# Kernel tuning notes

Hardware: AMD Instinct MI355X
Metric: run time of the kernel (lower is better)

The kernel has to match this reference:

```python
import jax, jax.numpy as jnp
from jax import lax
import numpy as np

B, S, V, C, H, Z, NSTEP = 256, 128, 128, 16, 1024, 256, 128
VC = V * C


def _gru_cell(x, h, Wih, Whh, bih, bhh):
    # torch GRUCell: gates ordered r, z, n along rows of (3H, in)
    gi = x @ Wih.T + bih
    gh = h @ Whh.T + bhh
    ir, iz, inn = jnp.split(gi, 3, axis=-1)
    hr, hz, hn = jnp.split(gh, 3, axis=-1)
    r = jax.nn.sigmoid(ir + hr)
    zg = jax.nn.sigmoid(iz + hz)
    n = jnp.tanh(inn + r * hn)
    return (1.0 - zg) * n + zg * h


def setup_inputs() -> dict:
    key = jax.random.key(0)
    ks = jax.random.split(key, 32)
    sc = 0.05
    p = lambda k, shape: (jax.random.normal(k, shape, jnp.float32) * sc)
    inp = {
        "x": jax.random.normal(ks[0], (B, V, S), jnp.float32),
        "noise": jax.random.normal(ks[1], (B, Z), jnp.float32),
        "gruf_Wih": p(ks[2], (3 * H, V)), "gruf_Whh": p(ks[3], (3 * H, H)),
        "gruf_bih": p(ks[4], (3 * H,)), "gruf_bhh": p(ks[5], (3 * H,)),
        "grub_Wih": p(ks[6], (3 * H, V)), "grub_Whh": p(ks[7], (3 * H, H)),
        "grub_bih": p(ks[8], (3 * H,)), "grub_bhh": p(ks[9], (3 * H,)),
        "Wmu": p(ks[10], (Z, 2 * H)), "bmu": p(ks[11], (Z,)),
        "Wvar": p(ks[12], (Z, 2 * H)), "bvar": p(ks[13], (Z,)),
        "Winit": p(ks[14], (H, Z)), "binit": p(ks[15], (H,)),
        "c1_Wih": p(ks[16], (3 * H, Z + VC)), "c1_Whh": p(ks[17], (3 * H, H)),
        "c1_bih": p(ks[18], (3 * H,)), "c1_bhh": p(ks[19], (3 * H,)),
        "c2_Wih": p(ks[20], (3 * H, H)), "c2_Whh": p(ks[21], (3 * H, H)),
        "c2_bih": p(ks[22], (3 * H,)), "c2_bhh": p(ks[23], (3 * H,)),
        "Wout": p(ks[24], (VC, H)), "bout": p(ks[25], (VC,)),
    }
    return inp


def reference(x, noise, gruf_Wih, gruf_Whh, gruf_bih, gruf_bhh,
              grub_Wih, grub_Whh, grub_bih, grub_bhh,
              Wmu, bmu, Wvar, bvar, Winit, binit,
              c1_Wih, c1_Whh, c1_bih, c1_bhh,
              c2_Wih, c2_Whh, c2_bih, c2_bhh, Wout, bout):
    b = x.shape[0]
    xe = jnp.transpose(x, (0, 2, 1))           # (b, s, V)
    xt = jnp.swapaxes(xe, 0, 1)                # (s, b, V) time-major
    h0 = jnp.zeros((b, H), x.dtype)

    def step_f(h, xs):
        h2 = _gru_cell(xs, h, gruf_Wih, gruf_Whh, gruf_bih, gruf_bhh)
        return h2, None

    def step_b(h, xs):
        h2 = _gru_cell(xs, h, grub_Wih, grub_Whh, grub_bih, grub_bhh)
        return h2, None

    hf, _ = lax.scan(step_f, h0, xt)
    hb, _ = lax.scan(step_b, h0, xt[::-1])
    enc = jnp.concatenate([hf, hb], axis=-1)   # (b, 2H) = h_n transposed+flattened

    mu = enc @ Wmu.T + bmu
    var = jnp.exp(enc @ Wvar.T + bvar)         # Normal(mu, var): var is the scale
    z = mu + var * noise                       # rsample

    out0 = jnp.zeros((b, VC), x.dtype).at[:, -1].set(1.0)
    h1_0 = jnp.tanh(z @ Winit.T + binit)
    h2_0 = jnp.zeros((b, H), x.dtype)

    def dstep(carry, i):
        out, h1, h2 = carry
        inp = jnp.concatenate([out, z], axis=1)          # (b, VC + Z)
        h1n = _gru_cell(inp, h1, c1_Wih, c1_Whh, c1_bih, c1_bhh)
        h2_prev = jnp.where(i == 0, h1n, h2)             # hx[1] = hx[0] at step 0
        h2n = _gru_cell(h1n, h2_prev, c2_Wih, c2_Whh, c2_bih, c2_bhh)
        logits = h2n @ Wout.T + bout                     # (b, VC)
        ls = jax.nn.log_softmax(logits.reshape(b, C, V), axis=1).reshape(b, VC)
        # eval-mode _sampling: argmax -> one-hot (no gradient flows through it)
        out_n = jax.nn.one_hot(jnp.argmax(ls, axis=1), VC, dtype=ls.dtype)
        return (out_n, h1n, h2n), ls

    _, xs = lax.scan(dstep, (out0, h1_0, h2_0), jnp.arange(NSTEP))
    recon_seq = jnp.swapaxes(xs, 0, 1)                   # (b, n_step, VC)
    recon = jnp.transpose(recon_seq, (0, 2, 1)).reshape(b, C, V, NSTEP)
    return mu, var, z, recon
```

## Files before the change

### kernel.cpp

```cpp
#include <hip/hip_runtime.h>
#include <cstdint>
#include <cstddef>

typedef __attribute__((ext_vector_type(8))) short bf16x8;
typedef __attribute__((ext_vector_type(4))) float f32x4;

#define DEVI __device__ __forceinline__

constexpr int B = 256, S = 128, V = 128, C = 16, H = 1024, Z = 256, NSTEP = 128;
constexpr int VC = V * C;
constexpr int G3 = 3 * H;

DEVI unsigned short f2bf(float f) {
  unsigned u = __float_as_uint(f);
  u += 0x7fffu + ((u >> 16) & 1u);
  return (unsigned short)(u >> 16);
}
DEVI float sigm(float x) { return 1.0f / (1.0f + expf(-x)); }

__global__ void k_cvt(const float* __restrict__ src, unsigned short* __restrict__ dst, int n) {
  for (int i = blockIdx.x * 256 + threadIdx.x; i < n; i += gridDim.x * 256)
    dst[i] = f2bf(src[i]);
}

__global__ void k_xt(const float* __restrict__ x, unsigned short* __restrict__ xtb) {
  __shared__ float tile[32][33];
  int sb = blockIdx.x * 32, rb = blockIdx.y * 32;
  int tx = threadIdx.x, ty = threadIdx.y;
  for (int i = ty; i < 32; i += 8) tile[i][tx] = x[(size_t)(rb + i) * S + sb + tx];
  __syncthreads();
  for (int i = ty; i < 32; i += 8)
    xtb[(size_t)(sb + i) * (B * V) + rb + tx] = f2bf(tile[tx][i]);
}

__global__ void k_wt(const float* __restrict__ w, float* __restrict__ wt) {
  __shared__ float tile[32][33];
  int vb = blockIdx.x * 32, nb = blockIdx.y * 32;
  int tx = threadIdx.x, ty = threadIdx.y;
  for (int i = ty; i < 32; i += 8) tile[i][tx] = w[(size_t)(nb + i) * (VC + Z) + vb + tx];
  __syncthreads();
  for (int i = ty; i < 32; i += 8)
    wt[(size_t)(vb + i) * G3 + nb + tx] = tile[tx][i];
}

struct GemmJob {
  const unsigned short* A;
  const unsigned short* Bw;
  float* Cm;
  int lda, ldb, ldc, K;
};
struct GemmJobs4 { GemmJob j[4]; };

typedef __attribute__((address_space(1))) const unsigned short* gas_p;
typedef __attribute__((address_space(3))) unsigned short* las_p;

__global__ __launch_bounds__(256) void k_gemm(GemmJobs4 jobs) {
  GemmJob jb = jobs.j[blockIdx.z];
  const int tid = threadIdx.x;
  const int wave = tid >> 6;
  const int lane = tid & 63;
  const int bn = blockIdx.x * 64;
  const int bm = blockIdx.y * 64;
  __shared__ unsigned short As[64 * 64];
  __shared__ unsigned short Bs[64 * 64];
  f32x4 acc[2][2] = {};
  const int wm = ((wave >> 1) & 1) * 32;
  const int wn = (wave & 1) * 32;
  const int rrow = (lane >> 3) & 7;
  const int pc = lane & 7;
  const int l15 = lane & 15;
  const int l4 = lane >> 4;

  const int nkt = jb.K >> 6;
  for (int kt = 0; kt < nkt; ++kt) {
    const int kbase = kt << 6;
    __syncthreads();
#pragma unroll
    for (int i = 0; i < 2; ++i) {
      int row = wave * 16 + i * 8 + rrow;
      int c = pc ^ (row & 7);
      const unsigned short* ga = jb.A + (size_t)(bm + row) * jb.lda + kbase + c * 8;
      __builtin_amdgcn_global_load_lds((gas_p)ga, (las_p)&As[(wave * 16 + i * 8) * 64], 16, 0, 0);
      const unsigned short* gb = jb.Bw + (size_t)(bn + row) * jb.ldb + kbase + c * 8;
      __builtin_amdgcn_global_load_lds((gas_p)gb, (las_p)&Bs[(wave * 16 + i * 8) * 64], 16, 0, 0);
    }
    __syncthreads();
#pragma unroll
    for (int kf = 0; kf < 2; ++kf) {
      int ch = (kf << 2) + l4;
      bf16x8 af[2], bfr[2];
#pragma unroll
      for (int mi = 0; mi < 2; ++mi) {
        int row = wm + mi * 16 + l15;
        af[mi] = *(const bf16x8*)&As[row * 64 + ((ch ^ (row & 7)) << 3)];
      }
#pragma unroll
      for (int ni = 0; ni < 2; ++ni) {
        int row = wn + ni * 16 + l15;
        bfr[ni] = *(const bf16x8*)&Bs[row * 64 + ((ch ^ (row & 7)) << 3)];
      }
#pragma unroll
      for (int mi = 0; mi < 2; ++mi)
#pragma unroll
        for (int ni = 0; ni < 2; ++ni)
          acc[mi][ni] = __builtin_amdgcn_mfma_f32_16x16x32_bf16(af[mi], bfr[ni], acc[mi][ni], 0, 0, 0);
    }
  }
#pragma unroll
  for (int mi = 0; mi < 2; ++mi)
#pragma unroll
    for (int ni = 0; ni < 2; ++ni) {
      int m0 = bm + wm + mi * 16 + l4 * 4;
      int n0 = bn + wn + ni * 16 + l15;
#pragma unroll
      for (int r = 0; r < 4; ++r)
        jb.Cm[(size_t)(m0 + r) * jb.ldc + n0] = acc[mi][ni][r];
    }
}

__global__ void k_enc_combine(const float* __restrict__ gif, const float* __restrict__ ghf,
                              const float* __restrict__ gib, const float* __restrict__ ghb,
                              const float* __restrict__ bihf, const float* __restrict__ bhhf,
                              const float* __restrict__ bihb, const float* __restrict__ bhhb,
                              float* __restrict__ hf, unsigned short* __restrict__ hfb,
                              float* __restrict__ hb, unsigned short* __restrict__ hbb) {
  int idx = blockIdx.x * 256 + threadIdx.x;
  int b = idx >> 10, jj = idx & (H - 1);
  const float *gi, *gh, *bih, *bhh; float* h; unsigned short* hB;
  if (blockIdx.y == 0) { gi = gif; gh = ghf; bih = bihf; bhh = bhhf; h = hf; hB = hfb; }
  else                 { gi = gib; gh = ghb; bih = bihb; bhh = bhhb; h = hb; hB = hbb; }
  int base = b * G3 + jj;
  float ir = gi[base] + bih[jj];
  float iz = gi[base + H] + bih[H + jj];
  float in_ = gi[base + 2 * H] + bih[2 * H + jj];
  float hr = gh[base] + bhh[jj];
  float hz = gh[base + H] + bhh[H + jj];
  float hn = gh[base + 2 * H] + bhh[2 * H + jj];
  float r = sigm(ir + hr);
  float zg = sigm(iz + hz);
  float n = tanhf(in_ + r * hn);
  float hnew = (1.f - zg) * n + zg * h[idx];
  h[idx] = hnew;
  hB[idx] = f2bf(hnew);
}

__global__ void k_combine1(const float* __restrict__ zpart, const float* __restrict__ WT,
                           const float* __restrict__ gh1, const float* __restrict__ bhh,
                           const int* __restrict__ idxb,
                           float* __restrict__ h1, unsigned short* __restrict__ h1b) {
  int idx = blockIdx.x * 256 + threadIdx.x;
  int b = idx >> 10, jj = idx & (H - 1);
  const float* wrow = WT + (size_t)idxb[b] * G3;
  int base = b * G3 + jj;
  float ir = zpart[base] + wrow[jj];
  float iz = zpart[base + H] + wrow[H + jj];
  float in_ = zpart[base + 2 * H] + wrow[2 * H + jj];
  float hr = gh1[base] + bhh[jj];
  float hz = gh1[base + H] + bhh[H + jj];
  float hn = gh1[base + 2 * H] + bhh[2 * H + jj];
  float r = sigm(ir + hr);
  float zg = sigm(iz + hz);
  float n = tanhf(in_ + r * hn);
  float hnew = (1.f - zg) * n + zg * h1[idx];
  h1[idx] = hnew;
  h1b[idx] = f2bf(hnew);
}

__global__ void k_combine2(const float* __restrict__ gi2, const float* __restrict__ gh2,
                           const float* __restrict__ bih, const float* __restrict__ bhh,
                           const float* __restrict__ h2prev,
                           float* __restrict__ h2, unsigned short* __restrict__ h2b) {
  int idx = blockIdx.x * 256 + threadIdx.x;
  int b = idx >> 10, jj = idx & (H - 1);
  int base = b * G3 + jj;
  float ir = gi2[base] + bih[jj];
  float iz = gi2[base + H] + bih[H + jj];
  float in_ = gi2[base + 2 * H] + bih[2 * H + jj];
  float hr = gh2[base] + bhh[jj];
  float hz = gh2[base + H] + bhh[H + jj];
  float hn = gh2[base + 2 * H] + bhh[2 * H + jj];
  float r = sigm(ir + hr);
  float zg = sigm(iz + hz);
  float n = tanhf(in_ + r * hn);
  float hnew = (1.f - zg) * n + zg * h2prev[idx];
  h2[idx] = hnew;
  h2b[idx] = f2bf(hnew);
}

__global__ __launch_bounds__(256) void k_mu_var_z(const float* __restrict__ hf, const float* __restrict__ hb,
                                                  const float* __restrict__ Wmu, const float* __restrict__ bmu,
                                                  const float* __restrict__ Wvar, const float* __restrict__ bvar,
                                                  const float* __restrict__ noise,
                                                  float* __restrict__ omu, float* __restrict__ ovar,
                                                  float* __restrict__ oz, float* __restrict__ zws) {
  __shared__ float e[2 * H];
  int b = blockIdx.x, t = threadIdx.x;
  for (int i = 0; i < 2 * H / 256; ++i) {
    int k = t + i * 256;
    e[k] = (k < H) ? hf[b * H + k] : hb[b * H + k - H];
  }
  __syncthreads();
  const float* wm = Wmu + (size_t)t * 2 * H;
  const float* wv = Wvar + (size_t)t * 2 * H;
  float am = bmu[t], av = bvar[t];
  for (int k = 0; k < 2 * H; ++k) { am += e[k] * wm[k]; av += e[k] * wv[k]; }
  float vv = expf(av);
  float zz = am + vv * noise[b * Z + t];
  omu[b * Z + t] = am; ovar[b * Z + t] = vv; oz[b * Z + t] = zz; zws[b * Z + t] = zz;
}

__global__ void k_zpart(const float* __restrict__ z, const float* __restrict__ c1Wih,
                        const float* __restrict__ bih, float* __restrict__ zpart) {
  int idx = blockIdx.x * 256 + threadIdx.x;
  int b = idx / G3, n = idx % G3;
  const float* w = c1Wih + (size_t)n * (VC + Z) + VC;
  const float* zr = z + b * Z;
  float a = bih[n];
  for (int k = 0; k < Z; ++k) a += zr[k] * w[k];
  zpart[idx] = a;
}

__global__ void k_h1init(const float* __restrict__ z, const float* __restrict__ Winit,
                         const float* __restrict__ binit,
                         float* __restrict__ h1, unsigned short* __restrict__ h1b,
                         int* __restrict__ idxb) {
  int idx = blockIdx.x * 256 + threadIdx.x;
  int b = idx >> 10, jj = idx & (H - 1);
  const float* w = Winit + (size_t)jj * Z;
  const float* zr = z + b * Z;
  float a = binit[jj];
  for (int k = 0; k < Z; ++k) a += zr[k] * w[k];
  float t = tanhf(a);
  h1[idx] = t; h1b[idx] = f2bf(t);
  if (idx < B) idxb[idx] = VC - 1;
}

__global__ __launch_bounds__(256) void k_softmax(const float* __restrict__ logits,
                                                 const float* __restrict__ bout,
                                                 float* __restrict__ lsbuf, int slot,
                                                 int* __restrict__ idxb) {
  int b = blockIdx.x, t = threadIdx.x;
  __shared__ float ls[VC];
  __shared__ float rv[256];
  __shared__ int ri[256];
  for (int i = 0; i < VC / 256; ++i) {
    int n = t + i * 256;
    ls[n] = logits[(size_t)b * VC + n] + bout[n];
  }
  __syncthreads();
  if (t < V) {
    float m = -1e30f;
    for (int c = 0; c < C; ++c) m = fmaxf(m, ls[c * V + t]);
    float s = 0.f;
    for (int c = 0; c < C; ++c) s += expf(ls[c * V + t] - m);
    float lse = m + logf(s);
    for (int c = 0; c < C; ++c) ls[c * V + t] -= lse;
  }
  __syncthreads();
  float bv = -1e30f; int bi = 0;
  for (int i = 0; i < VC / 256; ++i) {
    int n = i * 256 + t;
    float v = ls[n];
    if (v > bv) { bv = v; bi = n; }
  }
  rv[t] = bv; ri[t] = bi;
  __syncthreads();
  for (int s2 = 128; s2 > 0; s2 >>= 1) {
    if (t < s2) {
      float v2 = rv[t + s2]; int i2 = ri[t + s2];
      if (v2 > rv[t] || (v2 == rv[t] && i2 < ri[t])) { rv[t] = v2; ri[t] = i2; }
    }
    __syncthreads();
  }
  if (t == 0) idxb[b] = ri[0];
  float* dst = lsbuf + (size_t)slot * B * VC + (size_t)b * VC;
  for (int i = 0; i < VC / 256; ++i) { int n = t + i * 256; dst[n] = ls[n]; }
}

__global__ void k_flush(const float* __restrict__ lsbuf, float* __restrict__ recon, int t0) {
  int idx = blockIdx.x * 256 + threadIdx.x;
  float* dst = recon + (size_t)idx * NSTEP + t0;
#pragma unroll
  for (int j = 0; j < 16; ++j) dst[j] = lsbuf[(size_t)j * B * VC + idx];
}

extern "C" void kernel_launch(void* const* d_in, const int* in_sizes, int n_in,
                              void* d_out, int out_size, void* d_ws, size_t ws_size,
                              hipStream_t stream) {
  const float* x        = (const float*)d_in[0];
  const float* noise    = (const float*)d_in[1];
  const float* gruf_Wih = (const float*)d_in[2];
  const float* gruf_Whh = (const float*)d_in[3];
  const float* gruf_bih = (const float*)d_in[4];
  const float* gruf_bhh = (const float*)d_in[5];
  const float* grub_Wih = (const float*)d_in[6];
  const float* grub_Whh = (const float*)d_in[7];
  const float* grub_bih = (const float*)d_in[8];
  const float* grub_bhh = (const float*)d_in[9];
  const float* Wmu      = (const float*)d_in[10];
  const float* bmu      = (const float*)d_in[11];
  const float* Wvar     = (const float*)d_in[12];
  const float* bvar     = (const float*)d_in[13];
  const float* Winit    = (const float*)d_in[14];
  const float* binit    = (const float*)d_in[15];
  const float* c1_Wih   = (const float*)d_in[16];
  const float* c1_Whh   = (const float*)d_in[17];
  const float* c1_bih   = (const float*)d_in[18];
  const float* c1_bhh   = (const float*)d_in[19];
  const float* c2_Wih   = (const float*)d_in[20];
  const float* c2_Whh   = (const float*)d_in[21];
  const float* c2_bih   = (const float*)d_in[22];
  const float* c2_bhh   = (const float*)d_in[23];
  const float* Wout     = (const float*)d_in[24];
  const float* bout     = (const float*)d_in[25];

  float* omu = (float*)d_out;
  float* ovar = omu + B * Z;
  float* oz = ovar + B * Z;
  float* orecon = oz + B * Z;

  char* p = (char*)d_ws;
  auto carve = [&](size_t bytes) { char* r = p; p += (bytes + 255) & ~(size_t)255; return r; };
  unsigned short* wihf_b  = (unsigned short*)carve((size_t)G3 * V * 2);
  unsigned short* whhf_b  = (unsigned short*)carve((size_t)G3 * H * 2);
  unsigned short* wihb_b  = (unsigned short*)carve((size_t)G3 * V * 2);
  unsigned short* whhb_b  = (unsigned short*)carve((size_t)G3 * H * 2);
  unsigned short* wc1hh_b = (unsigned short*)carve((size_t)G3 * H * 2);
  unsigned short* wc2ih_b = (unsigned short*)carve((size_t)G3 * H * 2);
  unsigned short* wc2hh_b = (unsigned short*)carve((size_t)G3 * H * 2);
  unsigned short* wout_b  = (unsigned short*)carve((size_t)VC * H * 2);
  unsigned short* xtb     = (unsigned short*)carve((size_t)S * B * V * 2);
  unsigned short* hfb     = (unsigned short*)carve((size_t)B * H * 2);
  unsigned short* hbb     = (unsigned short*)carve((size_t)B * H * 2);
  unsigned short* h1b     = (unsigned short*)carve((size_t)B * H * 2);
  unsigned short* h2b     = (unsigned short*)carve((size_t)B * H * 2);
  float* WT     = (float*)carve((size_t)VC * G3 * 4);
  float* zpart  = (float*)carve((size_t)B * G3 * 4);
  float* g0     = (float*)carve((size_t)B * G3 * 4);
  float* g1     = (float*)carve((size_t)B * G3 * 4);
  float* g2     = (float*)carve((size_t)B * G3 * 4);
  float* g3     = (float*)carve((size_t)B * G3 * 4);
  float* hf     = (float*)carve((size_t)B * H * 4);
  float* hb     = (float*)carve((size_t)B * H * 4);
  float* h1     = (float*)carve((size_t)B * H * 4);
  float* h2     = (float*)carve((size_t)B * H * 4);
  float* zws    = (float*)carve((size_t)B * Z * 4);
  float* logits = (float*)carve((size_t)B * VC * 4);
  float* lsbuf  = (float*)carve((size_t)16 * B * VC * 4);
  int* idxb     = (int*)carve((size_t)B * 4);

  dim3 blk(256);

  auto cvt = [&](const float* s, unsigned short* d, int n) {
    int nb = (n + 255) / 256; if (nb > 2048) nb = 2048;
    k_cvt<<<nb, blk, 0, stream>>>(s, d, n);
  };
  cvt(gruf_Wih, wihf_b, G3 * V);
  cvt(gruf_Whh, whhf_b, G3 * H);
  cvt(grub_Wih, wihb_b, G3 * V);
  cvt(grub_Whh, whhb_b, G3 * H);
  cvt(c1_Whh, wc1hh_b, G3 * H);
  cvt(c2_Wih, wc2ih_b, G3 * H);
  cvt(c2_Whh, wc2hh_b, G3 * H);
  cvt(Wout, wout_b, VC * H);
  k_xt<<<dim3(S / 32, (B * V) / 32), dim3(32, 8), 0, stream>>>(x, xtb);
  k_wt<<<dim3(VC / 32, G3 / 32), dim3(32, 8), 0, stream>>>(c1_Wih, WT);

  hipMemsetAsync(hf, 0, (size_t)B * H * 4, stream);
  hipMemsetAsync(hb, 0, (size_t)B * H * 4, stream);
  hipMemsetAsync(hfb, 0, (size_t)B * H * 2, stream);
  hipMemsetAsync(hbb, 0, (size_t)B * H * 2, stream);

  for (int s = 0; s < S; ++s) {
    GemmJobs4 jj;
    jj.j[0] = { xtb + (size_t)s * B * V,           wihf_b, g0, V, V, G3, V };
    jj.j[1] = { hfb,                               whhf_b, g1, H, H, G3, H };
    jj.j[2] = { xtb + (size_t)(S - 1 - s) * B * V, wihb_b, g2, V, V, G3, V };
    jj.j[3] = { hbb,                               whhb_b, g3, H, H, G3, H };
    k_gemm<<<dim3(G3 / 64, B / 64, 4), blk, 0, stream>>>(jj);
    k_enc_combine<<<dim3(B * H / 256, 2), blk, 0, stream>>>(
        g0, g1, g2, g3, gruf_bih, gruf_bhh, grub_bih, grub_bhh, hf, hfb, hb, hbb);
  }

  k_mu_var_z<<<B, blk, 0, stream>>>(hf, hb, Wmu, bmu, Wvar, bvar, noise, omu, ovar, oz, zws);
  k_zpart<<<B * G3 / 256, blk, 0, stream>>>(zws, c1_Wih, c1_bih, zpart);
  k_h1init<<<B * H / 256, blk, 0, stream>>>(zws, Winit, binit, h1, h1b, idxb);

  for (int t = 0; t < NSTEP; ++t) {
    GemmJobs4 ja;
    ja.j[0] = { h1b, wc1hh_b, g0, H, H, G3, H };
    ja.j[1] = ja.j[0]; ja.j[2] = ja.j[0]; ja.j[3] = ja.j[0];
    k_gemm<<<dim3(G3 / 64, B / 64, 1), blk, 0, stream>>>(ja);
    k_combine1<<<B * H / 256, blk, 0, stream>>>(zpart, WT, g0, c1_bhh, idxb, h1, h1b);

    GemmJobs4 jc;
    jc.j[0] = { h1b,                     wc2ih_b, g1, H, H, G3, H };
    jc.j[1] = { (t == 0 ? h1b : h2b),    wc2hh_b, g2, H, H, G3, H };
    jc.j[2] = jc.j[0]; jc.j[3] = jc.j[0];
    k_gemm<<<dim3(G3 / 64, B / 64, 2), blk, 0, stream>>>(jc);
    k_combine2<<<B * H / 256, blk, 0, stream>>>(g1, g2, c2_bih, c2_bhh,
                                                (t == 0 ? h1 : h2), h2, h2b);

    GemmJobs4 jl;
    jl.j[0] = { h2b, wout_b, logits, H, H, VC, H };
    jl.j[1] = jl.j[0]; jl.j[2] = jl.j[0]; jl.j[3] = jl.j[0];
    k_gemm<<<dim3(VC / 64, B / 64, 1), blk, 0, stream>>>(jl);

    k_softmax<<<B, blk, 0, stream>>>(logits, bout, lsbuf, t & 15, idxb);
    if ((t & 15) == 15)
      k_flush<<<B * VC / 256, blk, 0, stream>>>(lsbuf, orecon, t - 15);
  }
}
```

Before: 9.030 ms.

## Replace per-step kernel launches with persistent encoder/decoder kernels using grid barriers

After: 25.87 ms. 186% more time.

```diff
diff --git a/kernel.cpp b/kernel.cpp
--- a/kernel.cpp
+++ b/kernel.cpp
@@ -4,284 +4,477 @@
 
 typedef __attribute__((ext_vector_type(8))) short bf16x8;
 typedef __attribute__((ext_vector_type(4))) float f32x4;
-
 #define DEVI __device__ __forceinline__
 
 constexpr int B = 256, S = 128, V = 128, C = 16, H = 1024, Z = 256, NSTEP = 128;
-constexpr int VC = V * C;
-constexpr int G3 = 3 * H;
-
-DEVI unsigned short f2bf(float f) {
-  unsigned u = __float_as_uint(f);
-  u += 0x7fffu + ((u >> 16) & 1u);
-  return (unsigned short)(u >> 16);
-}
-DEVI float sigm(float x) { return 1.0f / (1.0f + expf(-x)); }
-
-__global__ void k_cvt(const float* __restrict__ src, unsigned short* __restrict__ dst, int n) {
-  for (int i = blockIdx.x * 256 + threadIdx.x; i < n; i += gridDim.x * 256)
-    dst[i] = f2bf(src[i]);
-}
-
-__global__ void k_xt(const float* __restrict__ x, unsigned short* __restrict__ xtb) {
-  __shared__ float tile[32][33];
-  int sb = blockIdx.x * 32, rb = blockIdx.y * 32;
-  int tx = threadIdx.x, ty = threadIdx.y;
-  for (int i = ty; i < 32; i += 8) tile[i][tx] = x[(size_t)(rb + i) * S + sb + tx];
-  __syncthreads();
-  for (int i = ty; i < 32; i += 8)
-    xtb[(size_t)(sb + i) * (B * V) + rb + tx] = f2bf(tile[tx][i]);
-}
-
-__global__ void k_wt(const float* __restrict__ w, float* __restrict__ wt) {
-  __shared__ float tile[32][33];
-  int vb = blockIdx.x * 32, nb = blockIdx.y * 32;
-  int tx = threadIdx.x, ty = threadIdx.y;
-  for (int i = ty; i < 32; i += 8) tile[i][tx] = w[(size_t)(nb + i) * (VC + Z) + vb + tx];
-  __syncthreads();
-  for (int i = ty; i < 32; i += 8)
-    wt[(size_t)(vb + i) * G3 + nb + tx] = tile[tx][i];
-}
-
-struct GemmJob {
-  const unsigned short* A;
-  const unsigned short* Bw;
-  float* Cm;
-  int lda, ldb, ldc, K;
-};
-struct GemmJobs4 { GemmJob j[4]; };
+constexpr int VC = V * C, G3 = 3 * H;
 
 typedef __attribute__((address_space(1))) const unsigned short* gas_p;
 typedef __attribute__((address_space(3))) unsigned short* las_p;
 
-__global__ __launch_bounds__(256) void k_gemm(GemmJobs4 jobs) {
-  GemmJob jb = jobs.j[blockIdx.z];
-  const int tid = threadIdx.x;
-  const int wave = tid >> 6;
-  const int lane = tid & 63;
-  const int bn = blockIdx.x * 64;
-  const int bm = blockIdx.y * 64;
-  __shared__ unsigned short As[64 * 64];
-  __shared__ unsigned short Bs[64 * 64];
-  f32x4 acc[2][2] = {};
-  const int wm = ((wave >> 1) & 1) * 32;
-  const int wn = (wave & 1) * 32;
-  const int rrow = (lane >> 3) & 7;
-  const int pc = lane & 7;
-  const int l15 = lane & 15;
-  const int l4 = lane >> 4;
-
-  const int nkt = jb.K >> 6;
-  for (int kt = 0; kt < nkt; ++kt) {
-    const int kbase = kt << 6;
-    __syncthreads();
-#pragma unroll
-    for (int i = 0; i < 2; ++i) {
-      int row = wave * 16 + i * 8 + rrow;
-      int c = pc ^ (row & 7);
-      const unsigned short* ga = jb.A + (size_t)(bm + row) * jb.lda + kbase + c * 8;
-      __builtin_amdgcn_global_load_lds((gas_p)ga, (las_p)&As[(wave * 16 + i * 8) * 64], 16, 0, 0);
-      const unsigned short* gb = jb.Bw + (size_t)(bn + row) * jb.ldb + kbase + c * 8;
-      __builtin_amdgcn_global_load_lds((gas_p)gb, (las_p)&Bs[(wave * 16 + i * 8) * 64], 16, 0, 0);
-    }
-    __syncthreads();
-#pragma unroll
-    for (int kf = 0; kf < 2; ++kf) {
-      int ch = (kf << 2) + l4;
-      bf16x8 af[2], bfr[2];
-#pragma unroll
-      for (int mi = 0; mi < 2; ++mi) {
-        int row = wm + mi * 16 + l15;
-        af[mi] = *(const bf16x8*)&As[row * 64 + ((ch ^ (row & 7)) << 3)];
-      }
-#pragma unroll
-      for (int ni = 0; ni < 2; ++ni) {
-        int row = wn + ni * 16 + l15;
-        bfr[ni] = *(const bf16x8*)&Bs[row * 64 + ((ch ^ (row & 7)) << 3)];
-      }
-#pragma unroll
-      for (int mi = 0; mi < 2; ++mi)
-#pragma unroll
-        for (int ni = 0; ni < 2; ++ni)
-          acc[mi][ni] = __builtin_amdgcn_mfma_f32_16x16x32_bf16(af[mi], bfr[ni], acc[mi][ni], 0, 0, 0);
-    }
-  }
-#pragma unroll
-  for (int mi = 0; mi < 2; ++mi)
-#pragma unroll
-    for (int ni = 0; ni < 2; ++ni) {
-      int m0 = bm + wm + mi * 16 + l4 * 4;
-      int n0 = bn + wn + ni * 16 + l15;
-#pragma unroll
-      for (int r = 0; r < 4; ++r)
-        jb.Cm[(size_t)(m0 + r) * jb.ldc + n0] = acc[mi][ni][r];
-    }
-}
-
-__global__ void k_enc_combine(const float* __restrict__ gif, const float* __restrict__ ghf,
-                              const float* __restrict__ gib, const float* __restrict__ ghb,
-                              const float* __restrict__ bihf, const float* __restrict__ bhhf,
-                              const float* __restrict__ bihb, const float* __restrict__ bhhb,
-                              float* __restrict__ hf, unsigned short* __restrict__ hfb,
-                              float* __restrict__ hb, unsigned short* __restrict__ hbb) {
-  int idx = blockIdx.x * 256 + threadIdx.x;
-  int b = idx >> 10, jj = idx & (H - 1);
-  const float *gi, *gh, *bih, *bhh; float* h; unsigned short* hB;
-  if (blockIdx.y == 0) { gi = gif; gh = ghf; bih = bihf; bhh = bhhf; h = hf; hB = hfb; }
-  else                 { gi = gib; gh = ghb; bih = bihb; bhh = bhhb; h = hb; hB = hbb; }
-  int base = b * G3 + jj;
-  float ir = gi[base] + bih[jj];
-  float iz = gi[base + H] + bih[H + jj];
-  float in_ = gi[base + 2 * H] + bih[2 * H + jj];
-  float hr = gh[base] + bhh[jj];
-  float hz = gh[base + H] + bhh[H + jj];
-  float hn = gh[base + 2 * H] + bhh[2 * H + jj];
-  float r = sigm(ir + hr);
-  float zg = sigm(iz + hz);
-  float n = tanhf(in_ + r * hn);
-  float hnew = (1.f - zg) * n + zg * h[idx];
-  h[idx] = hnew;
-  hB[idx] = f2bf(hnew);
-}
-
-__global__ void k_combine1(const float* __restrict__ zpart, const float* __restrict__ WT,
-                           const float* __restrict__ gh1, const float* __restrict__ bhh,
-                           const int* __restrict__ idxb,
-                           float* __restrict__ h1, unsigned short* __restrict__ h1b) {
-  int idx = blockIdx.x * 256 + threadIdx.x;
-  int b = idx >> 10, jj = idx & (H - 1);
-  const float* wrow = WT + (size_t)idxb[b] * G3;
-  int base = b * G3 + jj;
-  float ir = zpart[base] + wrow[jj];
-  float iz = zpart[base + H] + wrow[H + jj];
-  float in_ = zpart[base + 2 * H] + wrow[2 * H + jj];
-  float hr = gh1[base] + bhh[jj];
-  float hz = gh1[base + H] + bhh[H + jj];
-  float hn = gh1[base + 2 * H] + bhh[2 * H + jj];
-  float r = sigm(ir + hr);
-  float zg = sigm(iz + hz);
-  float n = tanhf(in_ + r * hn);
-  float hnew = (1.f - zg) * n + zg * h1[idx];
-  h1[idx] = hnew;
-  h1b[idx] = f2bf(hnew);
-}
-
-__global__ void k_combine2(const float* __restrict__ gi2, const float* __restrict__ gh2,
-                           const float* __restrict__ bih, const float* __restrict__ bhh,
-                           const float* __restrict__ h2prev,
-                           float* __restrict__ h2, unsigned short* __restrict__ h2b) {
-  int idx = blockIdx.x * 256 + threadIdx.x;
-  int b = idx >> 10, jj = idx & (H - 1);
-  int base = b * G3 + jj;
-  float ir = gi2[base] + bih[jj];
-  float iz = gi2[base + H] + bih[H + jj];
-  float in_ = gi2[base + 2 * H] + bih[2 * H + jj];
-  float hr = gh2[base] + bhh[jj];
-  float hz = gh2[base + H] + bhh[H + jj];
-  float hn = gh2[base + 2 * H] + bhh[2 * H + jj];
-  float r = sigm(ir + hr);
-  float zg = sigm(iz + hz);
-  float n = tanhf(in_ + r * hn);
-  float hnew = (1.f - zg) * n + zg * h2prev[idx];
-  h2[idx] = hnew;
-  h2b[idx] = f2bf(hnew);
-}
-
-__global__ __launch_bounds__(256) void k_mu_var_z(const float* __restrict__ hf, const float* __restrict__ hb,
-                                                  const float* __restrict__ Wmu, const float* __restrict__ bmu,
-                                                  const float* __restrict__ Wvar, const float* __restrict__ bvar,
-                                                  const float* __restrict__ noise,
-                                                  float* __restrict__ omu, float* __restrict__ ovar,
-                                                  float* __restrict__ oz, float* __restrict__ zws) {
-  __shared__ float e[2 * H];
-  int b = blockIdx.x, t = threadIdx.x;
-  for (int i = 0; i < 2 * H / 256; ++i) {
-    int k = t + i * 256;
-    e[k] = (k < H) ? hf[b * H + k] : hb[b * H + k - H];
+DEVI unsigned short f2bf(float f){unsigned u=__float_as_uint(f);u+=0x7fffu+((u>>16)&1u);return (unsigned short)(u>>16);}
+DEVI float sigm(float x){return 1.f/(1.f+expf(-x));}
+DEVI f32x4 MFMA(bf16x8 a,bf16x8 b,f32x4 c){return __builtin_amdgcn_mfma_f32_16x16x32_bf16(a,b,c,0,0,0);}
+DEVI void stage16(const unsigned short* g, unsigned short* l){__builtin_amdgcn_global_load_lds((gas_p)g,(las_p)l,16,0,0);}
+
+DEVI void gbar(unsigned* cnt, unsigned nblk, unsigned& tgt){
+  __syncthreads();
+  if (threadIdx.x==0){
+    tgt += nblk;
+    __threadfence();
+    __hip_atomic_fetch_add(cnt,1u,__ATOMIC_RELEASE,__HIP_MEMORY_SCOPE_AGENT);
+    while (__hip_atomic_load(cnt,__ATOMIC_RELAXED,__HIP_MEMORY_SCOPE_AGENT) < tgt)
+      __builtin_amdgcn_s_sleep(1);
+    __threadfence();
   }
   __syncthreads();
-  const float* wm = Wmu + (size_t)t * 2 * H;
-  const float* wv = Wvar + (size_t)t * 2 * H;
-  float am = bmu[t], av = bvar[t];
-  for (int k = 0; k < 2 * H; ++k) { am += e[k] * wm[k]; av += e[k] * wv[k]; }
-  float vv = expf(av);
-  float zz = am + vv * noise[b * Z + t];
-  omu[b * Z + t] = am; ovar[b * Z + t] = vv; oz[b * Z + t] = zz; zws[b * Z + t] = zz;
-}
-
-__global__ void k_zpart(const float* __restrict__ z, const float* __restrict__ c1Wih,
-                        const float* __restrict__ bih, float* __restrict__ zpart) {
-  int idx = blockIdx.x * 256 + threadIdx.x;
-  int b = idx / G3, n = idx % G3;
-  const float* w = c1Wih + (size_t)n * (VC + Z) + VC;
-  const float* zr = z + b * Z;
-  float a = bih[n];
-  for (int k = 0; k < Z; ++k) a += zr[k] * w[k];
-  zpart[idx] = a;
-}
-
-__global__ void k_h1init(const float* __restrict__ z, const float* __restrict__ Winit,
+}
+
+__global__ void k_cvt(const float* __restrict__ src, unsigned short* __restrict__ dst, int n){
+  for (int i=blockIdx.x*256+threadIdx.x;i<n;i+=gridDim.x*256) dst[i]=f2bf(src[i]);
+}
+
+__global__ void k_xt(const float* __restrict__ x, unsigned short* __restrict__ xtb){
+  __shared__ float tile[32][33];
+  int sb=blockIdx.x*32, rb=blockIdx.y*32, tx=threadIdx.x, ty=threadIdx.y;
+  for (int i=ty;i<32;i+=8) tile[i][tx]=x[(size_t)(rb+i)*S+sb+tx];
+  __syncthreads();
+  for (int i=ty;i<32;i+=8) xtb[(size_t)(sb+i)*(B*V)+rb+tx]=f2bf(tile[tx][i]);
+}
+
+__global__ void k_wt(const float* __restrict__ w, float* __restrict__ wt){
+  __shared__ float tile[32][33];
+  int vb=blockIdx.x*32, nb=blockIdx.y*32, tx=threadIdx.x, ty=threadIdx.y;
+  for (int i=ty;i<32;i+=8) tile[i][tx]=w[(size_t)(nb+i)*(VC+Z)+vb+tx];
+  __syncthreads();
+  for (int i=ty;i<32;i+=8) wt[(size_t)(vb+i)*G3+nb+tx]=tile[tx][i];
+}
+
+__global__ __launch_bounds__(256) void k_mu_var_z(const float* __restrict__ hf,const float* __restrict__ hb,
+    const float* __restrict__ Wmu,const float* __restrict__ bmu,
+    const float* __restrict__ Wvar,const float* __restrict__ bvar,
+    const float* __restrict__ noise,
+    float* __restrict__ omu,float* __restrict__ ovar,float* __restrict__ oz,float* __restrict__ zws){
+  __shared__ float e[2*H];
+  int b=blockIdx.x, t=threadIdx.x;
+  for (int i=0;i<2*H/256;++i){int k=t+i*256; e[k]=(k<H)?hf[b*H+k]:hb[b*H+k-H];}
+  __syncthreads();
+  const float* wm=Wmu+(size_t)t*2*H; const float* wv=Wvar+(size_t)t*2*H;
+  float am=bmu[t], av=bvar[t];
+  for (int k=0;k<2*H;++k){am+=e[k]*wm[k];av+=e[k]*wv[k];}
+  float vv=expf(av), zz=am+vv*noise[b*Z+t];
+  omu[b*Z+t]=am; ovar[b*Z+t]=vv; oz[b*Z+t]=zz; zws[b*Z+t]=zz;
+}
+
+__global__ void k_zpart(const float* __restrict__ z,const float* __restrict__ c1Wih,
+                        const float* __restrict__ bih,float* __restrict__ zpart){
+  int idx=blockIdx.x*256+threadIdx.x;
+  int b=idx/G3, n=idx%G3;
+  const float* w=c1Wih+(size_t)n*(VC+Z)+VC;
+  const float* zr=z+b*Z;
+  float a=bih[n];
+  for (int k=0;k<Z;++k) a+=zr[k]*w[k];
+  zpart[idx]=a;
+}
+
+__global__ void k_h1init(const float* __restrict__ z,const float* __restrict__ Winit,
                          const float* __restrict__ binit,
-                         float* __restrict__ h1, unsigned short* __restrict__ h1b,
-                         int* __restrict__ idxb) {
-  int idx = blockIdx.x * 256 + threadIdx.x;
-  int b = idx >> 10, jj = idx & (H - 1);
-  const float* w = Winit + (size_t)jj * Z;
-  const float* zr = z + b * Z;
-  float a = binit[jj];
-  for (int k = 0; k < Z; ++k) a += zr[k] * w[k];
-  float t = tanhf(a);
-  h1[idx] = t; h1b[idx] = f2bf(t);
-  if (idx < B) idxb[idx] = VC - 1;
-}
-
-__global__ __launch_bounds__(256) void k_softmax(const float* __restrict__ logits,
-                                                 const float* __restrict__ bout,
-                                                 float* __restrict__ lsbuf, int slot,
-                                                 int* __restrict__ idxb) {
-  int b = blockIdx.x, t = threadIdx.x;
-  __shared__ float ls[VC];
-  __shared__ float rv[256];
-  __shared__ int ri[256];
-  for (int i = 0; i < VC / 256; ++i) {
-    int n = t + i * 256;
-    ls[n] = logits[(size_t)b * VC + n] + bout[n];
+                         float* __restrict__ h1f,unsigned short* __restrict__ h1b,int* __restrict__ idxb){
+  int idx=blockIdx.x*256+threadIdx.x;
+  int b=idx>>10, jj=idx&(H-1);
+  const float* w=Winit+(size_t)jj*Z;
+  const float* zr=z+b*Z;
+  float a=binit[jj];
+  for (int k=0;k<Z;++k) a+=zr[k]*w[k];
+  float t=tanhf(a);
+  h1f[idx]=t; h1b[idx]=f2bf(t);
+  if (idx<B) idxb[idx]=VC-1;
+}
+
+struct EncP {
+  const unsigned short *xtb,*wihf,*whhf,*wihb,*whhb;
+  const float *bihf,*bhhf,*bihb,*bhhb;
+  unsigned short *hfb0,*hfb1,*hbb0,*hbb1;
+  float *hf,*hb;
+  unsigned* bar;
+};
+
+__global__ __launch_bounds__(256,1) void k_enc(EncP P){
+  const int tid=threadIdx.x, wave=tid>>6, lane=tid&63;
+  const int l15=lane&15, l4=lane>>4, l8r=lane>>3, l8c=lane&7;
+  const int bid=blockIdx.x, xcd=bid&7, local=bid>>3;
+  const int mt=local>>2;
+  const int jgroup=(local&3)*8+xcd;
+  const int dir=jgroup>>4, jt=jgroup&15;
+  const unsigned short* wih=dir?P.wihb:P.wihf;
+  const unsigned short* whh=dir?P.whhb:P.whhf;
+  const float* bih=dir?P.bihb:P.bihf;
+  const float* bhh=dir?P.bhhb:P.bhhf;
+  unsigned short* hbuf[2]={dir?P.hbb0:P.hfb0, dir?P.hbb1:P.hfb1};
+  __shared__ unsigned short As[64*64];
+  __shared__ unsigned short Bs[3*64*64];
+  const int wm=(wave&1)*32, wn=(wave>>1)*32;
+  float bR[2],bZ[2],bN[2],hRb[2],hZb[2],hNb[2];
+#pragma unroll
+  for (int nf=0;nf<2;++nf){
+    int j=jt*64+wn+nf*16+l15;
+    bR[nf]=bih[j]; bZ[nf]=bih[H+j]; bN[nf]=bih[2*H+j];
+    hRb[nf]=bhh[j]; hZb[nf]=bhh[H+j]; hNb[nf]=bhh[2*H+j];
   }
-  __syncthreads();
-  if (t < V) {
-    float m = -1e30f;
-    for (int c = 0; c < C; ++c) m = fmaxf(m, ls[c * V + t]);
-    float s = 0.f;
-    for (int c = 0; c < C; ++c) s += expf(ls[c * V + t] - m);
-    float lse = m + logf(s);
-    for (int c = 0; c < C; ++c) ls[c * V + t] -= lse;
+  float hreg[2][2][4]={};
+  unsigned tgt=0;
+
+  for (int s=0;s<S;++s){
+    const unsigned short* hsrc=hbuf[s&1];
+    const int xs=dir?(S-1-s):s;
+    const unsigned short* xsrc=P.xtb+(size_t)xs*B*V;
+    f32x4 aR[2][2]={},aZ[2][2]={},aNH[2][2]={},aNX[2][2]={};
+    for (int kt=0;kt<16;++kt){
+      __syncthreads();
+#pragma unroll
+      for (int i=0;i<2;++i){
+        int seg=wave+i*4, row=seg*8+l8r, c=l8c^(row&7);
+        stage16(hsrc+(size_t)(mt*64+row)*H+kt*64+c*8, &As[seg*8*64]);
+      }
+#pragma unroll
+      for (int i=0;i<6;++i){
+        int seg=wave+i*4, row=seg*8+l8r, r=row&63, c=l8c^(r&7);
+        int wrow=(row>>6)*H+jt*64+r;
+        stage16(whh+(size_t)wrow*H+kt*64+c*8, &Bs[seg*8*64]);
+      }
+      __syncthreads();
+#pragma unroll
+      for (int kf=0;kf<2;++kf){
+        int ch=kf*4+l4;
+        bf16x8 a[2];
+#pragma unroll
+        for (int mi=0;mi<2;++mi){int ar=wm+mi*16+l15; a[mi]=*(const bf16x8*)&As[ar*64+((ch^(ar&7))<<3)];}
+#pragma unroll
+        for (int nf=0;nf<2;++nf){
+          int br=wn+nf*16+l15, off=(ch^(br&7))<<3;
+          bf16x8 b0=*(const bf16x8*)&Bs[br*64+off];
+          bf16x8 b1=*(const bf16x8*)&Bs[(64+br)*64+off];
+          bf16x8 b2=*(const bf16x8*)&Bs[(128+br)*64+off];
+#pragma unroll
+          for (int mi=0;mi<2;++mi){
+            aR[mi][nf]=MFMA(a[mi],b0,aR[mi][nf]);
+            aZ[mi][nf]=MFMA(a[mi],b1,aZ[mi][nf]);
+            aNH[mi][nf]=MFMA(a[mi],b2,aNH[mi][nf]);
+          }
+        }
+      }
+    }
+    for (int kt=0;kt<2;++kt){
+      __syncthreads();
+#pragma unroll
+      for (int i=0;i<2;++i){
+        int seg=wave+i*4, row=seg*8+l8r, c=l8c^(row&7);
+        stage16(xsrc+(size_t)(mt*64+row)*V+kt*64+c*8, &As[seg*8*64]);
+      }
+#pragma unroll
+      for (int i=0;i<6;++i){
+        int seg=wave+i*4, row=seg*8+l8r, r=row&63, c=l8c^(r&7);
+        int wrow=(row>>6)*H+jt*64+r;
+        stage16(wih+(size_t)wrow*V+kt*64+c*8, &Bs[seg*8*64]);
+      }
+      __syncthreads();
+#pragma unroll
+      for (int kf=0;kf<2;++kf){
+        int ch=kf*4+l4;
+        bf16x8 a[2];
+#pragma unroll
+        for (int mi=0;mi<2;++mi){int ar=wm+mi*16+l15; a[mi]=*(const bf16x8*)&As[ar*64+((ch^(ar&7))<<3)];}
+#pragma unroll
+        for (int nf=0;nf<2;++nf){
+          int br=wn+nf*16+l15, off=(ch^(br&7))<<3;
+          bf16x8 b0=*(const bf16x8*)&Bs[br*64+off];
+          bf16x8 b1=*(const bf16x8*)&Bs[(64+br)*64+off];
+          bf16x8 b2=*(const bf16x8*)&Bs[(128+br)*64+off];
+#pragma unroll
+          for (int mi=0;mi<2;++mi){
+            aR[mi][nf]=MFMA(a[mi],b0,aR[mi][nf]);
+            aZ[mi][nf]=MFMA(a[mi],b1,aZ[mi][nf]);
+            aNX[mi][nf]=MFMA(a[mi],b2,aNX[mi][nf]);
+          }
+        }
+      }
+    }
+    unsigned short* hdst=hbuf[(s+1)&1];
+#pragma unroll
+    for (int mi=0;mi<2;++mi)
+#pragma unroll
+      for (int nf=0;nf<2;++nf){
+        int j=jt*64+wn+nf*16+l15;
+#pragma unroll
+        for (int r4=0;r4<4;++r4){
+          int m=mt*64+wm+mi*16+l4*4+r4;
+          float rg=sigm(aR[mi][nf][r4]+bR[nf]+hRb[nf]);
+          float zg=sigm(aZ[mi][nf][r4]+bZ[nf]+hZb[nf]);
+          float nn=tanhf(aNX[mi][nf][r4]+bN[nf]+rg*(aNH[mi][nf][r4]+hNb[nf]));
+          float hnew=(1.f-zg)*nn+zg*hreg[mi][nf][r4];
+          hreg[mi][nf][r4]=hnew;
+          hdst[(size_t)m*H+j]=f2bf(hnew);
+        }
+      }
+    gbar(P.bar, gridDim.x, tgt);
   }
-  __syncthreads();
-  float bv = -1e30f; int bi = 0;
-  for (int i = 0; i < VC / 256; ++i) {
-    int n = i * 256 + t;
-    float v = ls[n];
-    if (v > bv) { bv = v; bi = n; }
+  float* hout=dir?P.hb:P.hf;
+#pragma unroll
+  for (int mi=0;mi<2;++mi)
+#pragma unroll
+    for (int nf=0;nf<2;++nf){
+      int j=jt*64+wn+nf*16+l15;
+#pragma unroll
+      for (int r4=0;r4<4;++r4){
+        int m=mt*64+wm+mi*16+l4*4+r4;
+        hout[(size_t)m*H+j]=hreg[mi][nf][r4];
+      }
+    }
+}
+
+struct DecP {
+  unsigned short *h1b0,*h1b1,*h2b0,*h2b1;
+  const unsigned short *w1hh,*w2ih,*w2hh,*wout;
+  const float *bhh1,*bih2,*bhh2,*bout;
+  const float *zpart,*WT,*h1f;
+  float *logits,*lsbuf,*recon;
+  int* idxb;
+  unsigned* bar;
+};
+
+__global__ __launch_bounds__(256,1) void k_dec(DecP P){
+  union SH {
+    struct { unsigned short A1[32*64]; unsigned short A2[32*64]; unsigned short Bt[6*64*64]; } g;
+    struct { float ls[VC]; float rv[256]; int ri[256]; } sm;
+  };
+  __shared__ SH u;
+  const int tid=threadIdx.x, wave=tid>>6, lane=tid&63;
+  const int l15=lane&15, l4=lane>>4, l8r=lane>>3, l8c=lane&7;
+  const int bid=blockIdx.x, xcd=bid&7, local=bid>>3;
+  const bool act12=(local<16);
+  const int jt=(local&1)*8+xcd;
+  const int mt=(local>>1)&7;
+  const int jt3=(local&3)*8+xcd;
+  const int mt3=local>>2;
+  const int wm=(wave&1)*16, wn=(wave>>1)*32;
+  unsigned short* h1b[2]={P.h1b0,P.h1b1};
+  unsigned short* h2b[2]={P.h2b0,P.h2b1};
+
+  float h1reg[2][4]={}, h2reg[2][4]={};
+  float zpR[2][4],zpZ[2][4],zpN[2][4];
+  float b1R[2],b1Z[2],b1N[2];
+  float c2R[2],c2Z[2],bi2N[2],bh2N[2];
+  float bo3[2];
+  if (act12){
+#pragma unroll
+    for (int nf=0;nf<2;++nf){
+      int j=jt*64+wn+nf*16+l15;
+      b1R[nf]=P.bhh1[j]; b1Z[nf]=P.bhh1[H+j]; b1N[nf]=P.bhh1[2*H+j];
+      c2R[nf]=P.bih2[j]+P.bhh2[j]; c2Z[nf]=P.bih2[H+j]+P.bhh2[H+j];
+      bi2N[nf]=P.bih2[2*H+j]; bh2N[nf]=P.bhh2[2*H+j];
+#pragma unroll
+      for (int r4=0;r4<4;++r4){
+        int m=mt*32+wm+l4*4+r4;
+        h1reg[nf][r4]=P.h1f[(size_t)m*H+j];
+        zpR[nf][r4]=P.zpart[(size_t)m*G3+j];
+        zpZ[nf][r4]=P.zpart[(size_t)m*G3+H+j];
+        zpN[nf][r4]=P.zpart[(size_t)m*G3+2*H+j];
+      }
+    }
   }
-  rv[t] = bv; ri[t] = bi;
-  __syncthreads();
-  for (int s2 = 128; s2 > 0; s2 >>= 1) {
-    if (t < s2) {
-      float v2 = rv[t + s2]; int i2 = ri[t + s2];
-      if (v2 > rv[t] || (v2 == rv[t] && i2 < ri[t])) { rv[t] = v2; ri[t] = i2; }
-    }
-    __syncthreads();
+#pragma unroll
+  for (int nf=0;nf<2;++nf) bo3[nf]=P.bout[jt3*64+wn+nf*16+l15];
+
+  unsigned tgt=0;
+  for (int t=0;t<NSTEP;++t){
+    const int cur=t&1, nxt=cur^1;
+    if (act12){
+      const unsigned short* h1src=h1b[cur];
+      f32x4 aR[2]={},aZ[2]={},aN[2]={};
+      for (int kt=0;kt<16;++kt){
+        __syncthreads();
+        { int row=wave*8+l8r, c=l8c^(row&7);
+          stage16(h1src+(size_t)(mt*32+row)*H+kt*64+c*8, &u.g.A1[wave*8*64]); }
+#pragma unroll
+        for (int i=0;i<6;++i){
+          int seg=wave+i*4, row=seg*8+l8r, r=row&63, c=l8c^(r&7);
+          int wrow=(row>>6)*H+jt*64+r;
+          stage16(P.w1hh+(size_t)wrow*H+kt*64+c*8, &u.g.Bt[seg*8*64]);
+        }
+        __syncthreads();
+#pragma unroll
+        for (int kf=0;kf<2;++kf){
+          int ch=kf*4+l4, ar=wm+l15;
+          bf16x8 a=*(const bf16x8*)&u.g.A1[ar*64+((ch^(ar&7))<<3)];
+#pragma unroll
+          for (int nf=0;nf<2;++nf){
+            int br=wn+nf*16+l15, off=(ch^(br&7))<<3;
+            bf16x8 b0=*(const bf16x8*)&u.g.Bt[br*64+off];
+            bf16x8 b1=*(const bf16x8*)&u.g.Bt[(64+br)*64+off];
+            bf16x8 b2=*(const bf16x8*)&u.g.Bt[(128+br)*64+off];
+            aR[nf]=MFMA(a,b0,aR[nf]); aZ[nf]=MFMA(a,b1,aZ[nf]); aN[nf]=MFMA(a,b2,aN[nf]);
+          }
+        }
+      }
+      int idxm[4];
+#pragma unroll
+      for (int r4=0;r4<4;++r4) idxm[r4]=P.idxb[mt*32+wm+l4*4+r4];
+      unsigned short* h1dst=h1b[nxt];
+#pragma unroll
+      for (int nf=0;nf<2;++nf){
+        int j=jt*64+wn+nf*16+l15;
+#pragma unroll
+        for (int r4=0;r4<4;++r4){
+          const float* wt=P.WT+(size_t)idxm[r4]*G3;
+          float rg=sigm(zpR[nf][r4]+wt[j]+aR[nf][r4]+b1R[nf]);
+          float zg=sigm(zpZ[nf][r4]+wt[H+j]+aZ[nf][r4]+b1Z[nf]);
+          float nn=tanhf(zpN[nf][r4]+wt[2*H+j]+rg*(aN[nf][r4]+b1N[nf]));
+          float hnew=(1.f-zg)*nn+zg*h1reg[nf][r4];
+          h1reg[nf][r4]=hnew;
+          int m=mt*32+wm+l4*4+r4;
+          h1dst[(size_t)m*H+j]=f2bf(hnew);
+        }
+      }
+    }
+    gbar(P.bar,256,tgt);
+    if (act12){
+      const unsigned short* a1src=h1b[nxt];
+      const unsigned short* a2src=(t==0)?h1b[nxt]:h2b[cur];
+      f32x4 aR[2]={},aZ[2]={},aNI[2]={},aNH[2]={};
+      for (int kt=0;kt<16;++kt){
+        __syncthreads();
+        { int row=wave*8+l8r, c=l8c^(row&7);
+          stage16(a1src+(size_t)(mt*32+row)*H+kt*64+c*8, &u.g.A1[wave*8*64]);
+          stage16(a2src+(size_t)(mt*32+row)*H+kt*64+c*8, &u.g.A2[wave*8*64]); }
+#pragma unroll
+        for (int i=0;i<12;++i){
+          int seg=wave+i*4, row=seg*8+l8r, g6=row>>6, r=row&63, c=l8c^(r&7);
+          const unsigned short* wsrc=(g6<3)?P.w2ih:P.w2hh;
+          int wrow=(g6%3)*H+jt*64+r;
+          stage16(wsrc+(size_t)wrow*H+kt*64+c*8, &u.g.Bt[seg*8*64]);
+        }
+        __syncthreads();
+#pragma unroll
+        for (int kf=0;kf<2;++kf){
+          int ch=kf*4+l4, ar=wm+l15, aoff=(ch^(ar&7))<<3;
+          bf16x8 a1=*(const bf16x8*)&u.g.A1[ar*64+aoff];
+          bf16x8 a2=*(const bf16x8*)&u.g.A2[ar*64+aoff];
+#pragma unroll
+          for (int nf=0;nf<2;++nf){
+            int br=wn+nf*16+l15, off=(ch^(br&7))<<3;
+            bf16x8 bri=*(const bf16x8*)&u.g.Bt[br*64+off];
+            bf16x8 bzi=*(const bf16x8*)&u.g.Bt[(64+br)*64+off];
+            bf16x8 bni=*(const bf16x8*)&u.g.Bt[(128+br)*64+off];
+            bf16x8 brh=*(const bf16x8*)&u.g.Bt[(192+br)*64+off];
+            bf16x8 bzh=*(const bf16x8*)&u.g.Bt[(256+br)*64+off];
+            bf16x8 bnh=*(const bf16x8*)&u.g.Bt[(320+br)*64+off];
+            aR[nf]=MFMA(a1,bri,aR[nf]); aR[nf]=MFMA(a2,brh,aR[nf]);
+            aZ[nf]=MFMA(a1,bzi,aZ[nf]); aZ[nf]=MFMA(a2,bzh,aZ[nf]);
+            aNI[nf]=MFMA(a1,bni,aNI[nf]); aNH[nf]=MFMA(a2,bnh,aNH[nf]);
+          }
+        }
+      }
+      unsigned short* h2dst=h2b[nxt];
+#pragma unroll
+      for (int nf=0;nf<2;++nf){
+        int j=jt*64+wn+nf*16+l15;
+#pragma unroll
+        for (int r4=0;r4<4;++r4){
+          float rg=sigm(aR[nf][r4]+c2R[nf]);
+          float zg=sigm(aZ[nf][r4]+c2Z[nf]);
+          float nn=tanhf(aNI[nf][r4]+bi2N[nf]+rg*(aNH[nf][r4]+bh2N[nf]));
+          float hp=(t==0)?h1reg[nf][r4]:h2reg[nf][r4];
+          float hnew=(1.f-zg)*nn+zg*hp;
+          h2reg[nf][r4]=hnew;
+          int m=mt*32+wm+l4*4+r4;
+          h2dst[(size_t)m*H+j]=f2bf(hnew);
+        }
+      }
+    }
+    gbar(P.bar,256,tgt);
+    {
+      const unsigned short* asrc=h2b[nxt];
+      f32x4 acc[2]={};
+      for (int kt=0;kt<16;++kt){
+        __syncthreads();
+        { int row=wave*8+l8r, c=l8c^(row&7);
+          stage16(asrc+(size_t)(mt3*32+row)*H+kt*64+c*8, &u.g.A1[wave*8*64]); }
+#pragma unroll
+        for (int i=0;i<2;++i){
+          int seg=wave+i*4, row=seg*8+l8r, c=l8c^(row&7);
+          int wrow=jt3*64+row;
+          stage16(P.wout+(size_t)wrow*H+kt*64+c*8, &u.g.Bt[seg*8*64]);
+        }
+        __syncthreads();
+#pragma unroll
+        for (int kf=0;kf<2;++kf){
+          int ch=kf*4+l4, ar=wm+l15;
+          bf16x8 a=*(const bf16x8*)&u.g.A1[ar*64+((ch^(ar&7))<<3)];
+#pragma unroll
+          for (int nf=0;nf<2;++nf){
+            int br=wn+nf*16+l15, off=(ch^(br&7))<<3;
+            bf16x8 b0=*(const bf16x8*)&u.g.Bt[br*64+off];
+            acc[nf]=MFMA(a,b0,acc[nf]);
+          }
+        }
+      }
+#pragma unroll
+      for (int nf=0;nf<2;++nf){
+        int n=jt3*64+wn+nf*16+l15;
+#pragma unroll
+        for (int r4=0;r4<4;++r4){
+          int m=mt3*32+wm+l4*4+r4;
+          P.logits[(size_t)m*VC+n]=acc[nf][r4]+bo3[nf];
+        }
+      }
+    }
+    gbar(P.bar,256,tgt);
+    {
+      const int b=bid;
+#pragma unroll
+      for (int i=0;i<VC/256;++i){int n=tid+i*256; u.sm.ls[n]=P.logits[(size_t)b*VC+n];}
+      __syncthreads();
+      if (tid<V){
+        float mx=-1e30f;
+        for (int c=0;c<C;++c) mx=fmaxf(mx,u.sm.ls[c*V+tid]);
+        float sum=0.f;
+        for (int c=0;c<C;++c) sum+=expf(u.sm.ls[c*V+tid]-mx);
+        float lse=mx+logf(sum);
+        for (int c=0;c<C;++c) u.sm.ls[c*V+tid]-=lse;
+      }
+      __syncthreads();
+      float bv=-1e30f; int bi=0;
+#pragma unroll
+      for (int i=0;i<VC/256;++i){
+        int n=i*256+tid; float v=u.sm.ls[n];
+        if (v>bv){bv=v;bi=n;}
+      }
+      u.sm.rv[tid]=bv; u.sm.ri[tid]=bi;
+      __syncthreads();
+      for (int s2=128;s2>0;s2>>=1){
+        if (tid<s2){
+          float v2=u.sm.rv[tid+s2]; int i2=u.sm.ri[tid+s2];
+          if (v2>u.sm.rv[tid]||(v2==u.sm.rv[tid]&&i2<u.sm.ri[tid])){u.sm.rv[tid]=v2;u.sm.ri[tid]=i2;}
+        }
+        __syncthreads();
+      }
+      if (tid==0) P.idxb[b]=u.sm.ri[0];
+      float* dst=P.lsbuf+(size_t)(t&15)*B*VC+(size_t)b*VC;
+#pragma unroll
+      for (int i=0;i<VC/256;++i){int n=tid+i*256; dst[n]=u.sm.ls[n];}
+    }
+    gbar(P.bar,256,tgt);
+    if ((t&15)==15){
+      int t0=t-15, base=bid*256+tid;
+#pragma unroll
+      for (int i=0;i<8;++i){
+        int e=base+i*65536;
+        float* dst=P.recon+(size_t)e*NSTEP+t0;
+#pragma unroll
+        for (int j2=0;j2<16;++j2) dst[j2]=P.lsbuf[(size_t)j2*B*VC+e];
+      }
+    }
   }
-  if (t == 0) idxb[b] = ri[0];
-  float* dst = lsbuf + (size_t)slot * B * VC + (size_t)b * VC;
-  for (int i = 0; i < VC / 256; ++i) { int n = t + i * 256; dst[n] = ls[n]; }
-}
-
-__global__ void k_flush(const float* __restrict__ lsbuf, float* __restrict__ recon, int t0) {
-  int idx = blockIdx.x * 256 + threadIdx.x;
-  float* dst = recon + (size_t)idx * NSTEP + t0;
-#pragma unroll
-  for (int j = 0; j < 16; ++j) dst[j] = lsbuf[(size_t)j * B * VC + idx];
 }
 
 extern "C" void kernel_launch(void* const* d_in, const int* in_sizes, int n_in,
@@ -315,99 +508,76 @@
   const float* bout     = (const float*)d_in[25];
 
   float* omu = (float*)d_out;
-  float* ovar = omu + B * Z;
-  float* oz = ovar + B * Z;
-  float* orecon = oz + B * Z;
+  float* ovar = omu + B*Z;
+  float* oz = ovar + B*Z;
+  float* orecon = oz + B*Z;
 
   char* p = (char*)d_ws;
-  auto carve = [&](size_t bytes) { char* r = p; p += (bytes + 255) & ~(size_t)255; return r; };
-  unsigned short* wihf_b  = (unsigned short*)carve((size_t)G3 * V * 2);
-  unsigned short* whhf_b  = (unsigned short*)carve((size_t)G3 * H * 2);
-  unsigned short* wihb_b  = (unsigned short*)carve((size_t)G3 * V * 2);
-  unsigned short* whhb_b  = (unsigned short*)carve((size_t)G3 * H * 2);
-  unsigned short* wc1hh_b = (unsigned short*)carve((size_t)G3 * H * 2);
-  unsigned short* wc2ih_b = (unsigned short*)carve((size_t)G3 * H * 2);
-  unsigned short* wc2hh_b = (unsigned short*)carve((size_t)G3 * H * 2);
-  unsigned short* wout_b  = (unsigned short*)carve((size_t)VC * H * 2);
-  unsigned short* xtb     = (unsigned short*)carve((size_t)S * B * V * 2);
-  unsigned short* hfb     = (unsigned short*)carve((size_t)B * H * 2);
-  unsigned short* hbb     = (unsigned short*)carve((size_t)B * H * 2);
-  unsigned short* h1b     = (unsigned short*)carve((size_t)B * H * 2);
-  unsigned short* h2b     = (unsigned short*)carve((size_t)B * H * 2);
-  float* WT     = (float*)carve((size_t)VC * G3 * 4);
-  float* zpart  = (float*)carve((size_t)B * G3 * 4);
-  float* g0     = (float*)carve((size_t)B * G3 * 4);
-  float* g1     = (float*)carve((size_t)B * G3 * 4);
-  float* g2     = (float*)carve((size_t)B * G3 * 4);
-  float* g3     = (float*)carve((size_t)B * G3 * 4);
-  float* hf     = (float*)carve((size_t)B * H * 4);
-  float* hb     = (float*)carve((size_t)B * H * 4);
-  float* h1     = (float*)carve((size_t)B * H * 4);
-  float* h2     = (float*)carve((size_t)B * H * 4);
-  float* zws    = (float*)carve((size_t)B * Z * 4);
-  float* logits = (float*)carve((size_t)B * VC * 4);
-  float* lsbuf  = (float*)carve((size_t)16 * B * VC * 4);
-  int* idxb     = (int*)carve((size_t)B * 4);
+  auto carve = [&](size_t bytes){ char* r = p; p += (bytes+255)&~(size_t)255; return r; };
+  unsigned short* wihf_b  = (unsigned short*)carve((size_t)G3*V*2);
+  unsigned short* whhf_b  = (unsigned short*)carve((size_t)G3*H*2);
+  unsigned short* wihb_b  = (unsigned short*)carve((size_t)G3*V*2);
+  unsigned short* whhb_b  = (unsigned short*)carve((size_t)G3*H*2);
+  unsigned short* wc1hh_b = (unsigned short*)carve((size_t)G3*H*2);
+  unsigned short* wc2ih_b = (unsigned short*)carve((size_t)G3*H*2);
+  unsigned short* wc2hh_b = (unsigned short*)carve((size_t)G3*H*2);
+  unsigned short* wout_b  = (unsigned short*)carve((size_t)VC*H*2);
+  unsigned short* xtb     = (unsigned short*)carve((size_t)S*B*V*2);
+  unsigned short* hfb0    = (unsigned short*)carve((size_t)B*H*2);
+  unsigned short* hfb1    = (unsigned short*)carve((size_t)B*H*2);
+  unsigned short* hbb0    = (unsigned short*)carve((size_t)B*H*2);
+  unsigned short* hbb1    = (unsigned short*)carve((size_t)B*H*2);
+  unsigned short* h1b0    = (unsigned short*)carve((size_t)B*H*2);
+  unsigned short* h1b1    = (unsigned short*)carve((size_t)B*H*2);
+  unsigned short* h2b0    = (unsigned short*)carve((size_t)B*H*2);
+  unsigned short* h2b1    = (unsigned short*)carve((size_t)B*H*2);
+  float* WT     = (float*)carve((size_t)VC*G3*4);
+  float* zpart  = (float*)carve((size_t)B*G3*4);
+  float* hf     = (float*)carve((size_t)B*H*4);
+  float* hb     = (float*)carve((size_t)B*H*4);
+  float* h1f    = (float*)carve((size_t)B*H*4);
+  float* zws    = (float*)carve((size_t)B*Z*4);
+  float* logits = (float*)carve((size_t)B*VC*4);
+  float* lsbuf  = (float*)carve((size_t)16*B*VC*4);
+  int* idxb     = (int*)carve((size_t)B*4);
+  unsigned* bars= (unsigned*)carve(2*sizeof(unsigned));
 
   dim3 blk(256);
-
-  auto cvt = [&](const float* s, unsigned short* d, int n) {
-    int nb = (n + 255) / 256; if (nb > 2048) nb = 2048;
-    k_cvt<<<nb, blk, 0, stream>>>(s, d, n);
+  auto cvt=[&](const float* s, unsigned short* d, int n){
+    int nb=(n+255)/256; if (nb>2048) nb=2048;
+    k_cvt<<<nb,blk,0,stream>>>(s,d,n);
   };
-  cvt(gruf_Wih, wihf_b, G3 * V);
-  cvt(gruf_Whh, whhf_b, G3 * H);
-  cvt(grub_Wih, wihb_b, G3 * V);
-  cvt(grub_Whh, whhb_b, G3 * H);
-  cvt(c1_Whh, wc1hh_b, G3 * H);
-  cvt(c2_Wih, wc2ih_b, G3 * H);
-  cvt(c2_Whh, wc2hh_b, G3 * H);
-  cvt(Wout, wout_b, VC * H);
-  k_xt<<<dim3(S / 32, (B * V) / 32), dim3(32, 8), 0, stream>>>(x, xtb);
-  k_wt<<<dim3(VC / 32, G3 / 32), dim3(32, 8), 0, stream>>>(c1_Wih, WT);
-
-  hipMemsetAsync(hf, 0, (size_t)B * H * 4, stream);
-  hipMemsetAsync(hb, 0, (size_t)B * H * 4, stream);
-  hipMemsetAsync(hfb, 0, (size_t)B * H * 2, stream);
-  hipMemsetAsync(hbb, 0, (size_t)B * H * 2, stream);
-
-  for (int s = 0; s < S; ++s) {
-    GemmJobs4 jj;
-    jj.j[0] = { xtb + (size_t)s * B * V,           wihf_b, g0, V, V, G3, V };
-    jj.j[1] = { hfb,                               whhf_b, g1, H, H, G3, H };
-    jj.j[2] = { xtb + (size_t)(S - 1 - s) * B * V, wihb_b, g2, V, V, G3, V };
-    jj.j[3] = { hbb,                               whhb_b, g3, H, H, G3, H };
-    k_gemm<<<dim3(G3 / 64, B / 64, 4), blk, 0, stream>>>(jj);
-    k_enc_combine<<<dim3(B * H / 256, 2), blk, 0, stream>>>(
-        g0, g1, g2, g3, gruf_bih, gruf_bhh, grub_bih, grub_bhh, hf, hfb, hb, hbb);
-  }
-
-  k_mu_var_z<<<B, blk, 0, stream>>>(hf, hb, Wmu, bmu, Wvar, bvar, noise, omu, ovar, oz, zws);
-  k_zpart<<<B * G3 / 256, blk, 0, stream>>>(zws, c1_Wih, c1_bih, zpart);
-  k_h1init<<<B * H / 256, blk, 0, stream>>>(zws, Winit, binit, h1, h1b, idxb);
-
-  for (int t = 0; t < NSTEP; ++t) {
-    GemmJobs4 ja;
-    ja.j[0] = { h1b, wc1hh_b, g0, H, H, G3, H };
-    ja.j[1] = ja.j[0]; ja.j[2] = ja.j[0]; ja.j[3] = ja.j[0];
-    k_gemm<<<dim3(G3 / 64, B / 64, 1), blk, 0, stream>>>(ja);
-    k_combine1<<<B * H / 256, blk, 0, stream>>>(zpart, WT, g0, c1_bhh, idxb, h1, h1b);
-
-    GemmJobs4 jc;
-    jc.j[0] = { h1b,                     wc2ih_b, g1, H, H, G3, H };
-    jc.j[1] = { (t == 0 ? h1b : h2b),    wc2hh_b, g2, H, H, G3, H };
-    jc.j[2] = jc.j[0]; jc.j[3] = jc.j[0];
-    k_gemm<<<dim3(G3 / 64, B / 64, 2), blk, 0, stream>>>(jc);
-    k_combine2<<<B * H / 256, blk, 0, stream>>>(g1, g2, c2_bih, c2_bhh,
-                                                (t == 0 ? h1 : h2), h2, h2b);
-
-    GemmJobs4 jl;
-    jl.j[0] = { h2b, wout_b, logits, H, H, VC, H };
-    jl.j[1] = jl.j[0]; jl.j[2] = jl.j[0]; jl.j[3] = jl.j[0];
-    k_gemm<<<dim3(VC / 64, B / 64, 1), blk, 0, stream>>>(jl);
-
-    k_softmax<<<B, blk, 0, stream>>>(logits, bout, lsbuf, t & 15, idxb);
-    if ((t & 15) == 15)
-      k_flush<<<B * VC / 256, blk, 0, stream>>>(lsbuf, orecon, t - 15);
-  }
-}
+  cvt(gruf_Wih,wihf_b,G3*V);
+  cvt(gruf_Whh,whhf_b,G3*H);
+  cvt(grub_Wih,wihb_b,G3*V);
+  cvt(grub_Whh,whhb_b,G3*H);
+  cvt(c1_Whh,wc1hh_b,G3*H);
+  cvt(c2_Wih,wc2ih_b,G3*H);
+  cvt(c2_Whh,wc2hh_b,G3*H);
+  cvt(Wout,wout_b,VC*H);
+  k_xt<<<dim3(S/32,(B*V)/32),dim3(32,8),0,stream>>>(x,xtb);
+  k_wt<<<dim3(VC/32,G3/32),dim3(32,8),0,stream>>>(c1_Wih,WT);
+  hipMemsetAsync(hfb0,0,(size_t)B*H*2,stream);
+  hipMemsetAsync(hbb0,0,(size_t)B*H*2,stream);
+  hipMemsetAsync(bars,0,2*sizeof(unsigned),stream);
+
+  EncP ep;
+  ep.xtb=xtb; ep.wihf=wihf_b; ep.whhf=whhf_b; ep.wihb=wihb_b; ep.whhb=whhb_b;
+  ep.bihf=gruf_bih; ep.bhhf=gruf_bhh; ep.bihb=grub_bih; ep.bhhb=grub_bhh;
+  ep.hfb0=hfb0; ep.hfb1=hfb1; ep.hbb0=hbb0; ep.hbb1=hbb1;
+  ep.hf=hf; ep.hb=hb; ep.bar=bars;
+  k_enc<<<128,blk,0,stream>>>(ep);
+
+  k_mu_var_z<<<B,blk,0,stream>>>(hf,hb,Wmu,bmu,Wvar,bvar,noise,omu,ovar,oz,zws);
+  k_zpart<<<B*G3/256,blk,0,stream>>>(zws,c1_Wih,c1_bih,zpart);
+  k_h1init<<<B*H/256,blk,0,stream>>>(zws,Winit,binit,h1f,h1b0,idxb);
+
+  DecP dp;
+  dp.h1b0=h1b0; dp.h1b1=h1b1; dp.h2b0=h2b0; dp.h2b1=h2b1;
+  dp.w1hh=wc1hh_b; dp.w2ih=wc2ih_b; dp.w2hh=wc2hh_b; dp.wout=wout_b;
+  dp.bhh1=c1_bhh; dp.bih2=c2_bih; dp.bhh2=c2_bhh; dp.bout=bout;
+  dp.zpart=zpart; dp.WT=WT; dp.h1f=h1f;
+  dp.logits=logits; dp.lsbuf=lsbuf; dp.recon=orecon;
+  dp.idxb=idxb; dp.bar=bars+1;
+  k_dec<<<256,blk,0,stream>>>(dp);
+}
```
